# Optimization experiments

Measured on AMD Instinct MI355X. Metric: run time of the kernel, lower is better.

Reference implementation:

```python
import jax, jax.numpy as jnp
import numpy as np

EPS = 1e-5

def _layernorm(x, g, b):
    mu = jnp.mean(x, axis=-1, keepdims=True)
    var = jnp.var(x, axis=-1, keepdims=True)
    return (x - mu) * jax.lax.rsqrt(var + EPS) * g + b

def _pos_encoding(S, D, dtype):
    pos = jnp.arange(S, dtype=jnp.float32)[:, None]
    div = jnp.exp(jnp.arange(0, D, 2, dtype=jnp.float32) * (-jnp.log(10000.0) / D))
    pe = jnp.zeros((S, D), dtype=jnp.float32)
    pe = pe.at[:, 0::2].set(jnp.sin(pos * div))
    pe = pe.at[:, 1::2].set(jnp.cos(pos * div))
    return pe.astype(dtype)

def setup_inputs() -> dict:
    key = jax.random.key(0)
    B, S, D, H, F, L = 4, 1024, 768, 12, 3072, 6
    ks = jax.random.split(key, 8)
    s = 0.02
    return {
        "x": jax.random.normal(ks[0], (B, S, D), jnp.float32),
        "Wqkv": jax.random.normal(ks[1], (L, D, 3 * D), jnp.float32) * s,
        "bqkv": jnp.zeros((L, 3 * D), jnp.float32),
        "Wo": jax.random.normal(ks[2], (L, D, D), jnp.float32) * s,
        "bo": jnp.zeros((L, D), jnp.float32),
        "ln1_g": jnp.ones((L, D), jnp.float32),
        "ln1_b": jnp.zeros((L, D), jnp.float32),
        "W1": jax.random.normal(ks[3], (L, D, F), jnp.float32) * s,
        "b1": jnp.zeros((L, F), jnp.float32),
        "W2": jax.random.normal(ks[4], (L, F, D), jnp.float32) * s,
        "b2": jnp.zeros((L, D), jnp.float32),
        "ln2_g": jnp.ones((L, D), jnp.float32),
        "ln2_b": jnp.zeros((L, D), jnp.float32),
        "lnf_g": jnp.ones((D,), jnp.float32),
        "lnf_b": jnp.zeros((D,), jnp.float32),
        "num_heads": 12,
    }

def reference(x, Wqkv, bqkv, Wo, bo, ln1_g, ln1_b, W1, b1, W2, b2, ln2_g, ln2_b, lnf_g, lnf_b, num_heads):
    B, S, D = x.shape
    H = num_heads
    hd = D // H
    scale = 1.0 / jnp.sqrt(jnp.float32(hd)).astype(x.dtype)

    x = x + _pos_encoding(S, D, x.dtype)[None]

    def layer(h, params):
        wqkv, bq, wo, bo_, g1, b1_, w1, bias1, w2, bias2, g2, b2_ = params
        qkv = (h @ wqkv + bq).reshape(B, S, 3, H, hd)
        q, k, v = jnp.moveaxis(qkv, 2, 0)          # each [B,S,H,hd]
        q = q.transpose(0, 2, 1, 3)                 # bhqd
        k = k.transpose(0, 2, 1, 3)
        v = v.transpose(0, 2, 1, 3)
        scores = jnp.einsum('bhqd,bhkd->bhqk', q, k) * scale
        w = jax.nn.softmax(scores, axis=-1)
        w = jnp.clip(w, 1e-6, 1.0)                  # clamp as in torch module
        attn = jnp.einsum('bhqk,bhkd->bhqd', w, v)
        attn = attn.transpose(0, 2, 1, 3).reshape(B, S, D) @ wo + bo_
        h = _layernorm(h + attn, g1, b1_)
        ffn = jax.nn.relu(h @ w1 + bias1) @ w2 + bias2
        h = _layernorm(h + ffn, g2, b2_)
        return h, None

    params = (Wqkv, bqkv, Wo, bo, ln1_g, ln1_b, W1, b1, W2, b2, ln2_g, ln2_b)
    x, _ = jax.lax.scan(layer, x, params)
    return _layernorm(x, lnf_g, lnf_b)
```

## Files before the change

kernel.cpp:

```cpp
#include <hip/hip_runtime.h>
#include <math.h>

typedef float f32x4 __attribute__((ext_vector_type(4)));
typedef __bf16 bf16x8 __attribute__((ext_vector_type(8)));
typedef unsigned short u16x8 __attribute__((ext_vector_type(8)));

__device__ __forceinline__ unsigned short f2bf(float f) {
    union { float f; unsigned int u; } v; v.f = f;
    unsigned int r = v.u + 0x7FFFu + ((v.u >> 16) & 1u);
    return (unsigned short)(r >> 16);
}
__device__ __forceinline__ float bf2f(unsigned short u) {
    union { unsigned int u; float f; } v; v.u = ((unsigned int)u) << 16;
    return v.f;
}
__device__ __forceinline__ bf16x8 ld8(const unsigned short* p) {
    union { u16x8 u; bf16x8 b; } c;
    c.u = *(const u16x8*)p;
    return c.b;
}
__device__ __forceinline__ void gload_lds16(const unsigned short* g, unsigned short* l) {
    __builtin_amdgcn_global_load_lds(
        (const __attribute__((address_space(1))) unsigned int*)g,
        (__attribute__((address_space(3))) unsigned int*)l,
        16, 0, 0);
}
__device__ __forceinline__ int swz_off(int row, int quad) {
    return row * 32 + ((quad ^ ((row >> 1) & 3)) << 3);
}

__global__ __launch_bounds__(256)
void transpose_convert(const float* __restrict__ W, unsigned short* __restrict__ Wt,
                       int K, int N) {
    __shared__ float tile[32][33];
    int n0 = blockIdx.x * 32, k0 = blockIdx.y * 32;
    int tx = threadIdx.x & 31, ty = threadIdx.x >> 5;
#pragma unroll
    for (int i = 0; i < 4; ++i) {
        int k = ty + i * 8;
        tile[k][tx] = W[(size_t)(k0 + k) * N + n0 + tx];
    }
    __syncthreads();
#pragma unroll
    for (int i = 0; i < 4; ++i) {
        int n = ty + i * 8;
        Wt[(size_t)(n0 + n) * K + k0 + tx] = f2bf(tile[tx][n]);
    }
}

__global__ __launch_bounds__(256)
void posenc_k(const float* __restrict__ x, float* __restrict__ h,
              unsigned short* __restrict__ hb) {
    int idx = blockIdx.x * 256 + threadIdx.x;
    const int TOT = 4 * 1024 * 768;
    if (idx >= TOT) return;
    int d = idx % 768;
    int s = (idx / 768) % 1024;
    int i2 = d >> 1;
    float dv = expf(-(float)(2 * i2) * (9.210340371976184f / 768.0f));
    float ang = (float)s * dv;
    float pe = (d & 1) ? cosf(ang) : sinf(ang);
    float v = x[idx] + pe;
    h[idx] = v;
    hb[idx] = f2bf(v);
}

template<int WF32, int WBF16, int RELU, int BIAS>
__global__ __launch_bounds__(256)
void gemm_k(const unsigned short* __restrict__ A, const unsigned short* __restrict__ Bt,
            const float* __restrict__ bias, float* __restrict__ Cf,
            unsigned short* __restrict__ Cb, int M, int N, int K, int Kc) {
    __shared__ unsigned short As[128 * 32];
    __shared__ unsigned short Bs[128 * 32];
    const int tid = threadIdx.x;
    const int lane = tid & 63, wave = tid >> 6;
    const int l15 = lane & 15, quad = lane >> 4;
    const int m0 = blockIdx.y * 128, n0 = blockIdx.x * 128;
    const int wr = (wave >> 1) * 64, wc = (wave & 1) * 64;
    const int kstart = blockIdx.z * Kc, kend = kstart + Kc;
    float* Cfp = Cf + (size_t)blockIdx.z * M * N;

    const int r0 = wave * 32 + (lane >> 2);
    const int kc0 = lane & 3;

    f32x4 acc[4][4];
#pragma unroll
    for (int i = 0; i < 4; ++i)
#pragma unroll
        for (int j = 0; j < 4; ++j) acc[i][j] = (f32x4){0.f, 0.f, 0.f, 0.f};

    for (int k0 = kstart; k0 < kend; k0 += 32) {
        __syncthreads();
#pragma unroll
        for (int j = 0; j < 2; ++j) {
            int r = r0 + j * 16;
            int kcl = kc0 ^ ((r >> 1) & 3);
            const unsigned short* ga = A + (size_t)(m0 + r) * K + k0 + kcl * 8;
            const unsigned short* gb = Bt + (size_t)(n0 + r) * K + k0 + kcl * 8;
            gload_lds16(ga, &As[(wave * 32 + j * 16) * 32]);
            gload_lds16(gb, &Bs[(wave * 32 + j * 16) * 32]);
        }
        __syncthreads();
        bf16x8 af[4], bfr[4];
#pragma unroll
        for (int mt = 0; mt < 4; ++mt)
            af[mt] = ld8(&As[swz_off(wr + mt * 16 + l15, quad)]);
#pragma unroll
        for (int nt = 0; nt < 4; ++nt)
            bfr[nt] = ld8(&Bs[swz_off(wc + nt * 16 + l15, quad)]);
#pragma unroll
        for (int mt = 0; mt < 4; ++mt)
#pragma unroll
            for (int nt = 0; nt < 4; ++nt)
                acc[mt][nt] = __builtin_amdgcn_mfma_f32_16x16x32_bf16(
                    af[mt], bfr[nt], acc[mt][nt], 0, 0, 0);
    }
#pragma unroll
    for (int mt = 0; mt < 4; ++mt)
#pragma unroll
        for (int nt = 0; nt < 4; ++nt)
#pragma unroll
            for (int r = 0; r < 4; ++r) {
                int row = m0 + wr + mt * 16 + quad * 4 + r;
                int col = n0 + wc + nt * 16 + l15;
                float v = acc[mt][nt][r];
                if (BIAS) v += bias[col];
                if (RELU) v = fmaxf(v, 0.f);
                if (WF32) Cfp[(size_t)row * N + col] = v;
                if (WBF16) Cb[(size_t)row * N + col] = f2bf(v);
            }
}

__global__ __launch_bounds__(256)
void qksplit_k(const unsigned short* __restrict__ qkv, unsigned short* __restrict__ Q,
               unsigned short* __restrict__ Ko) {
    int o8 = blockIdx.x * 256 + threadIdx.x;
    const int NQ8 = 393216;
    int which = (o8 >= NQ8) ? 1 : 0;
    int oo = o8 - which * NQ8;
    int dg = (oo & 7) * 8;
    int s = (oo >> 3) & 1023;
    int bh = oo >> 13;
    int h = bh % 12, b = bh / 12;
    size_t row = (size_t)(b * 1024 + s);
    int col = which * 768 + h * 64 + dg;
    u16x8 val = *(const u16x8*)&qkv[row * 2304 + col];
    if (!which) {
#pragma unroll
        for (int j = 0; j < 8; ++j) val[j] = f2bf(bf2f(val[j]) * 0.125f);
        *(u16x8*)&Q[((size_t)bh * 1024 + s) * 64 + dg] = val;
    } else {
        *(u16x8*)&Ko[((size_t)bh * 1024 + s) * 64 + dg] = val;
    }
}

__global__ __launch_bounds__(256)
void vt_k(const unsigned short* __restrict__ qkv, unsigned short* __restrict__ Vt) {
    __shared__ unsigned short t[64][65];
    int bh = blockIdx.y, s0 = blockIdx.x * 64;
    int b = bh / 12, h = bh % 12;
    int tx = threadIdx.x & 63;
    int ty = threadIdx.x >> 6;
#pragma unroll
    for (int r = 0; r < 16; ++r) {
        int i = ty + r * 4;
        t[i][tx] = qkv[(size_t)(b * 1024 + s0 + i) * 2304 + 1536 + h * 64 + tx];
    }
    __syncthreads();
#pragma unroll
    for (int r = 0; r < 16; ++r) {
        int dd = ty + r * 4;
        Vt[((size_t)bh * 64 + dd) * 1024 + s0 + tx] = t[tx][dd];
    }
}

#define PSTR 68
__global__ __launch_bounds__(256)
void flash_k(const unsigned short* __restrict__ Q, const unsigned short* __restrict__ K,
             const unsigned short* __restrict__ Vt, unsigned short* __restrict__ ctx) {
    const int S = 1024, HD = 64;
    int bh = blockIdx.y;
    int b = bh / 12, h = bh % 12;
    int q0 = blockIdx.x * 64;
    const unsigned short* Qp = Q + ((size_t)bh * S + q0) * HD;
    const unsigned short* Kp = K + (size_t)bh * S * HD;
    const unsigned short* Vp = Vt + (size_t)bh * HD * S;

    __shared__ unsigned short Qs[128 * 32];
    __shared__ unsigned short Ks[128 * 32];
    __shared__ unsigned short Vs[128 * 32];
    __shared__ unsigned short Ps[4 * 16 * PSTR];

    int tid = threadIdx.x;
    int lane = tid & 63, wave = tid >> 6;
    int l15 = lane & 15, quad = lane >> 4;

    const int rl0 = lane >> 2;
    const int c0 = lane & 3;

#pragma unroll
    for (int j = 0; j < 2; ++j) {
        int R = wave * 32 + j * 16 + rl0;
        int khalf = R >> 6, grow = R & 63;
        int lch = c0 ^ ((R >> 1) & 3);
        gload_lds16(Qp + grow * HD + khalf * 32 + lch * 8,
                    &Qs[(wave * 32 + j * 16) * 32]);
    }

    f32x4 o[4];
#pragma unroll
    for (int i = 0; i < 4; ++i) o[i] = (f32x4){0.f, 0.f, 0.f, 0.f};
    float lsum[4] = {0.f, 0.f, 0.f, 0.f};

    unsigned short* Pw = &Ps[wave * 16 * PSTR];

    for (int kt = 0; kt < 16; ++kt) {
        __syncthreads();
#pragma unroll
        for (int j = 0; j < 2; ++j) {
            int R = wave * 32 + j * 16 + rl0;
            int khalf = R >> 6, grow = R & 63;
            int lch = c0 ^ ((R >> 1) & 3);
            gload_lds16(Kp + (kt * 64 + grow) * HD + khalf * 32 + lch * 8,
                        &Ks[(wave * 32 + j * 16) * 32]);
            gload_lds16(Vp + (size_t)grow * S + kt * 64 + khalf * 32 + lch * 8,
                        &Vs[(wave * 32 + j * 16) * 32]);
        }
        __syncthreads();

        bf16x8 qa0 = ld8(&Qs[swz_off(wave * 16 + l15, quad)]);
        bf16x8 qa1 = ld8(&Qs[swz_off(64 + wave * 16 + l15, quad)]);
        f32x4 sc[4];
#pragma unroll
        for (int cb = 0; cb < 4; ++cb) {
            bf16x8 kb0 = ld8(&Ks[swz_off(cb * 16 + l15, quad)]);
            bf16x8 kb1 = ld8(&Ks[swz_off(64 + cb * 16 + l15, quad)]);
            f32x4 z = (f32x4){0.f, 0.f, 0.f, 0.f};
            z = __builtin_amdgcn_mfma_f32_16x16x32_bf16(qa0, kb0, z, 0, 0, 0);
            z = __builtin_amdgcn_mfma_f32_16x16x32_bf16(qa1, kb1, z, 0, 0, 0);
            sc[cb] = z;
        }
#pragma unroll
        for (int cb = 0; cb < 4; ++cb)
#pragma unroll
            for (int r = 0; r < 4; ++r) {
                float pv = __expf(sc[cb][r]);
                sc[cb][r] = pv;
                lsum[r] += pv;
            }
#pragma unroll
        for (int cb = 0; cb < 4; ++cb)
#pragma unroll
            for (int r = 0; r < 4; ++r)
                Pw[(quad * 4 + r) * PSTR + cb * 16 + l15] = f2bf(sc[cb][r]);
        bf16x8 pa0 = ld8(&Pw[l15 * PSTR + quad * 8]);
        bf16x8 pa1 = ld8(&Pw[l15 * PSTR + 32 + quad * 8]);
#pragma unroll
        for (int cb = 0; cb < 4; ++cb) {
            bf16x8 vb0 = ld8(&Vs[swz_off(cb * 16 + l15, quad)]);
            bf16x8 vb1 = ld8(&Vs[swz_off(64 + cb * 16 + l15, quad)]);
            o[cb] = __builtin_amdgcn_mfma_f32_16x16x32_bf16(pa0, vb0, o[cb], 0, 0, 0);
            o[cb] = __builtin_amdgcn_mfma_f32_16x16x32_bf16(pa1, vb1, o[cb], 0, 0, 0);
        }
    }
#pragma unroll
    for (int r = 0; r < 4; ++r) {
#pragma unroll
        for (int off = 1; off < 16; off <<= 1) lsum[r] += __shfl_xor(lsum[r], off);
    }
#pragma unroll
    for (int cb = 0; cb < 4; ++cb)
#pragma unroll
        for (int r = 0; r < 4; ++r) {
            int row = q0 + wave * 16 + quad * 4 + r;
            float val = o[cb][r] / lsum[r];
            ctx[((size_t)(b * 1024 + row)) * 768 + h * 64 + cb * 16 + l15] = f2bf(val);
        }
}

template<int NPART, int WBF16>
__global__ __launch_bounds__(256)
void ln_k(const float* __restrict__ X, const float* __restrict__ P,
          const float* __restrict__ pb,
          const float* __restrict__ g, const float* __restrict__ bta,
          float* __restrict__ Yf, unsigned short* __restrict__ Yb) {
    const int D = 768;
    const size_t MD = (size_t)4096 * 768;
    int row = blockIdx.x;
    int tid = threadIdx.x;
    const float* x = X + (size_t)row * D;
    float v[3];
    float s = 0.f, s2 = 0.f;
#pragma unroll
    for (int i = 0; i < 3; ++i) {
        int c = i * 256 + tid;
        float t = x[c];
        if (NPART > 0) {
            float r = pb[c];
#pragma unroll
            for (int pi = 0; pi < NPART; ++pi)
                r += P[MD * pi + (size_t)row * D + c];
            t += r;
        }
        v[i] = t;
        s += t;
        s2 += t * t;
    }
#pragma unroll
    for (int off = 1; off < 64; off <<= 1) {
        s += __shfl_xor(s, off);
        s2 += __shfl_xor(s2, off);
    }
    __shared__ float rs[4], rs2[4];
    int wave = tid >> 6, lane = tid & 63;
    if (lane == 0) { rs[wave] = s; rs2[wave] = s2; }
    __syncthreads();
    s = rs[0] + rs[1] + rs[2] + rs[3];
    s2 = rs2[0] + rs2[1] + rs2[2] + rs2[3];
    float mu = s * (1.f / 768.f);
    float var = s2 * (1.f / 768.f) - mu * mu;
    float rstd = rsqrtf(var + 1e-5f);
#pragma unroll
    for (int i = 0; i < 3; ++i) {
        int c = i * 256 + tid;
        float y = (v[i] - mu) * rstd * g[c] + bta[c];
        Yf[(size_t)row * D + c] = y;
        if (WBF16) Yb[(size_t)row * D + c] = f2bf(y);
    }
}

extern "C" void kernel_launch(void* const* d_in, const int* in_sizes, int n_in,
                              void* d_out, int out_size, void* d_ws, size_t ws_size,
                              hipStream_t stream) {
    const float* x    = (const float*)d_in[0];
    const float* Wqkv = (const float*)d_in[1];
    const float* bqkv = (const float*)d_in[2];
    const float* Wo   = (const float*)d_in[3];
    const float* bo   = (const float*)d_in[4];
    const float* ln1g = (const float*)d_in[5];
    const float* ln1b = (const float*)d_in[6];
    const float* W1   = (const float*)d_in[7];
    const float* b1   = (const float*)d_in[8];
    const float* W2   = (const float*)d_in[9];
    const float* b2   = (const float*)d_in[10];
    const float* ln2g = (const float*)d_in[11];
    const float* ln2b = (const float*)d_in[12];
    const float* lnfg = (const float*)d_in[13];
    const float* lnfb = (const float*)d_in[14];

    const int B = 4, S = 1024, D = 768, H = 12, F = 3072, L = 6;
    const int M = B * S;

    char* p = (char*)d_ws;
    auto alloc = [&](size_t bytes) -> char* {
        char* r = p;
        p += (bytes + 255) & ~(size_t)255;
        return r;
    };
    float* h             = (float*)alloc((size_t)M * D * 4);
    float* tmp           = (float*)alloc((size_t)4 * M * D * 4);
    unsigned short* hb   = (unsigned short*)alloc((size_t)M * D * 2);
    unsigned short* act  = (unsigned short*)alloc((size_t)M * F * 2);
    unsigned short* Qb   = (unsigned short*)alloc((size_t)M * D * 2);
    unsigned short* Kb   = (unsigned short*)alloc((size_t)M * D * 2);
    unsigned short* Vtb  = (unsigned short*)alloc((size_t)M * D * 2);
    unsigned short* ctx  = (unsigned short*)alloc((size_t)M * D * 2);
    unsigned short* wqkvT = (unsigned short*)alloc((size_t)3 * D * D * 2);
    unsigned short* woT   = (unsigned short*)alloc((size_t)D * D * 2);
    unsigned short* w1T   = (unsigned short*)alloc((size_t)D * F * 2);
    unsigned short* w2T   = (unsigned short*)alloc((size_t)D * F * 2);
    unsigned short* qkvb = act;
    unsigned short* f1b  = act;

    posenc_k<<<(M * D) / 256, 256, 0, stream>>>(x, h, hb);

    for (int l = 0; l < L; ++l) {
        transpose_convert<<<dim3(3 * D / 32, D / 32), 256, 0, stream>>>(
            Wqkv + (size_t)l * D * 3 * D, wqkvT, D, 3 * D);
        transpose_convert<<<dim3(D / 32, D / 32), 256, 0, stream>>>(
            Wo + (size_t)l * D * D, woT, D, D);
        transpose_convert<<<dim3(F / 32, D / 32), 256, 0, stream>>>(
            W1 + (size_t)l * D * F, w1T, D, F);
        transpose_convert<<<dim3(D / 32, F / 32), 256, 0, stream>>>(
            W2 + (size_t)l * F * D, w2T, F, D);

        gemm_k<0, 1, 0, 1><<<dim3(3 * D / 128, M / 128, 1), 256, 0, stream>>>(
            hb, wqkvT, bqkv + (size_t)l * 3 * D, nullptr, qkvb, M, 3 * D, D, D);
        qksplit_k<<<786432 / 256, 256, 0, stream>>>(qkvb, Qb, Kb);
        vt_k<<<dim3(S / 64, B * H), 256, 0, stream>>>(qkvb, Vtb);
        flash_k<<<dim3(S / 64, B * H), 256, 0, stream>>>(Qb, Kb, Vtb, ctx);
        gemm_k<1, 0, 0, 0><<<dim3(D / 128, M / 128, 2), 256, 0, stream>>>(
            ctx, woT, nullptr, tmp, nullptr, M, D, D, D / 2);
        ln_k<2, 1><<<M, 256, 0, stream>>>(h, tmp, bo + (size_t)l * D,
                                          ln1g + (size_t)l * D, ln1b + (size_t)l * D,
                                          h, hb);
        gemm_k<0, 1, 1, 1><<<dim3(F / 128, M / 128, 1), 256, 0, stream>>>(
            hb, w1T, b1 + (size_t)l * F, nullptr, f1b, M, F, D, D);
        gemm_k<1, 0, 0, 0><<<dim3(D / 128, M / 128, 4), 256, 0, stream>>>(
            f1b, w2T, nullptr, tmp, nullptr, M, D, F, F / 4);
        ln_k<4, 1><<<M, 256, 0, stream>>>(h, tmp, b2 + (size_t)l * D,
                                          ln2g + (size_t)l * D, ln2b + (size_t)l * D,
                                          h, hb);
    }
    ln_k<0, 0><<<M, 256, 0, stream>>>(h, nullptr, nullptr, lnfg, lnfb,
                                      (float*)d_out, nullptr);
}
```

Before: 1.393 ms.

## Double-buffer LDS in GEMM and flash attention, store split-K partials as bf16

Adds two-stage LDS double buffering to the GEMM and flash-attention kernels so the next tile's global-to-LDS loads are issued before computing the current tile, with one barrier per iteration. Split-K partial outputs are now written in bf16 instead of fp32, halving partial-sum traffic read by the layernorm kernels. The Wo projection split-K is raised from 2 to 4 for more blocks. This doubles LDS use per block, possibly lowering occupancy, and reduces precision of the residual partial sums.

```diff
diff --git a/kernel.cpp b/kernel.cpp
--- a/kernel.cpp
+++ b/kernel.cpp
@@ -65,49 +65,56 @@
     hb[idx] = f2bf(v);
 }
 
-template<int WF32, int WBF16, int RELU, int BIAS>
+template<int RELU, int BIAS>
 __global__ __launch_bounds__(256)
 void gemm_k(const unsigned short* __restrict__ A, const unsigned short* __restrict__ Bt,
-            const float* __restrict__ bias, float* __restrict__ Cf,
-            unsigned short* __restrict__ Cb, int M, int N, int K, int Kc) {
-    __shared__ unsigned short As[128 * 32];
-    __shared__ unsigned short Bs[128 * 32];
+            const float* __restrict__ bias, unsigned short* __restrict__ Cb,
+            int M, int N, int K, int Kc) {
+    __shared__ unsigned short As[2][128 * 32];
+    __shared__ unsigned short Bs[2][128 * 32];
     const int tid = threadIdx.x;
     const int lane = tid & 63, wave = tid >> 6;
     const int l15 = lane & 15, quad = lane >> 4;
     const int m0 = blockIdx.y * 128, n0 = blockIdx.x * 128;
     const int wr = (wave >> 1) * 64, wc = (wave & 1) * 64;
-    const int kstart = blockIdx.z * Kc, kend = kstart + Kc;
-    float* Cfp = Cf + (size_t)blockIdx.z * M * N;
+    const int kstart = blockIdx.z * Kc;
+    unsigned short* Cbp = Cb + (size_t)blockIdx.z * M * N;
 
     const int r0 = wave * 32 + (lane >> 2);
     const int kc0 = lane & 3;
 
-    f32x4 acc[4][4];
-#pragma unroll
-    for (int i = 0; i < 4; ++i)
-#pragma unroll
-        for (int j = 0; j < 4; ++j) acc[i][j] = (f32x4){0.f, 0.f, 0.f, 0.f};
-
-    for (int k0 = kstart; k0 < kend; k0 += 32) {
-        __syncthreads();
+    auto stage = [&](int k0, int bi) {
 #pragma unroll
         for (int j = 0; j < 2; ++j) {
             int r = r0 + j * 16;
             int kcl = kc0 ^ ((r >> 1) & 3);
-            const unsigned short* ga = A + (size_t)(m0 + r) * K + k0 + kcl * 8;
-            const unsigned short* gb = Bt + (size_t)(n0 + r) * K + k0 + kcl * 8;
-            gload_lds16(ga, &As[(wave * 32 + j * 16) * 32]);
-            gload_lds16(gb, &Bs[(wave * 32 + j * 16) * 32]);
-        }
+            gload_lds16(A + (size_t)(m0 + r) * K + k0 + kcl * 8,
+                        &As[bi][(wave * 32 + j * 16) * 32]);
+            gload_lds16(Bt + (size_t)(n0 + r) * K + k0 + kcl * 8,
+                        &Bs[bi][(wave * 32 + j * 16) * 32]);
+        }
+    };
+
+    f32x4 acc[4][4];
+#pragma unroll
+    for (int i = 0; i < 4; ++i)
+#pragma unroll
+        for (int j = 0; j < 4; ++j) acc[i][j] = (f32x4){0.f, 0.f, 0.f, 0.f};
+
+    stage(kstart, 0);
+    const int nk = Kc / 32;
+    for (int t = 0; t < nk; ++t) {
         __syncthreads();
+        if (t + 1 < nk) stage(kstart + (t + 1) * 32, (t + 1) & 1);
+        const unsigned short* Asb = As[t & 1];
+        const unsigned short* Bsb = Bs[t & 1];
         bf16x8 af[4], bfr[4];
 #pragma unroll
         for (int mt = 0; mt < 4; ++mt)
-            af[mt] = ld8(&As[swz_off(wr + mt * 16 + l15, quad)]);
+            af[mt] = ld8(&Asb[swz_off(wr + mt * 16 + l15, quad)]);
 #pragma unroll
         for (int nt = 0; nt < 4; ++nt)
-            bfr[nt] = ld8(&Bs[swz_off(wc + nt * 16 + l15, quad)]);
+            bfr[nt] = ld8(&Bsb[swz_off(wc + nt * 16 + l15, quad)]);
 #pragma unroll
         for (int mt = 0; mt < 4; ++mt)
 #pragma unroll
@@ -126,8 +133,7 @@
                 float v = acc[mt][nt][r];
                 if (BIAS) v += bias[col];
                 if (RELU) v = fmaxf(v, 0.f);
-                if (WF32) Cfp[(size_t)row * N + col] = v;
-                if (WBF16) Cb[(size_t)row * N + col] = f2bf(v);
+                Cbp[(size_t)row * N + col] = f2bf(v);
             }
 }
 
@@ -187,8 +193,8 @@
     const unsigned short* Vp = Vt + (size_t)bh * HD * S;
 
     __shared__ unsigned short Qs[128 * 32];
-    __shared__ unsigned short Ks[128 * 32];
-    __shared__ unsigned short Vs[128 * 32];
+    __shared__ unsigned short Ks[2][128 * 32];
+    __shared__ unsigned short Vs[2][128 * 32];
     __shared__ unsigned short Ps[4 * 16 * PSTR];
 
     int tid = threadIdx.x;
@@ -197,6 +203,19 @@
 
     const int rl0 = lane >> 2;
     const int c0 = lane & 3;
+
+    auto stageKV = [&](int kt, int bi) {
+#pragma unroll
+        for (int j = 0; j < 2; ++j) {
+            int R = wave * 32 + j * 16 + rl0;
+            int khalf = R >> 6, grow = R & 63;
+            int lch = c0 ^ ((R >> 1) & 3);
+            gload_lds16(Kp + (kt * 64 + grow) * HD + khalf * 32 + lch * 8,
+                        &Ks[bi][(wave * 32 + j * 16) * 32]);
+            gload_lds16(Vp + (size_t)grow * S + kt * 64 + khalf * 32 + lch * 8,
+                        &Vs[bi][(wave * 32 + j * 16) * 32]);
+        }
+    };
 
 #pragma unroll
     for (int j = 0; j < 2; ++j) {
@@ -206,6 +225,7 @@
         gload_lds16(Qp + grow * HD + khalf * 32 + lch * 8,
                     &Qs[(wave * 32 + j * 16) * 32]);
     }
+    stageKV(0, 0);
 
     f32x4 o[4];
 #pragma unroll
@@ -216,25 +236,17 @@
 
     for (int kt = 0; kt < 16; ++kt) {
         __syncthreads();
-#pragma unroll
-        for (int j = 0; j < 2; ++j) {
-            int R = wave * 32 + j * 16 + rl0;
-            int khalf = R >> 6, grow = R & 63;
-            int lch = c0 ^ ((R >> 1) & 3);
-            gload_lds16(Kp + (kt * 64 + grow) * HD + khalf * 32 + lch * 8,
-                        &Ks[(wave * 32 + j * 16) * 32]);
-            gload_lds16(Vp + (size_t)grow * S + kt * 64 + khalf * 32 + lch * 8,
-                        &Vs[(wave * 32 + j * 16) * 32]);
-        }
-        __syncthreads();
+        if (kt < 15) stageKV(kt + 1, (kt + 1) & 1);
+        const unsigned short* Ksb = Ks[kt & 1];
+        const unsigned short* Vsb = Vs[kt & 1];
 
         bf16x8 qa0 = ld8(&Qs[swz_off(wave * 16 + l15, quad)]);
         bf16x8 qa1 = ld8(&Qs[swz_off(64 + wave * 16 + l15, quad)]);
         f32x4 sc[4];
 #pragma unroll
         for (int cb = 0; cb < 4; ++cb) {
-            bf16x8 kb0 = ld8(&Ks[swz_off(cb * 16 + l15, quad)]);
-            bf16x8 kb1 = ld8(&Ks[swz_off(64 + cb * 16 + l15, quad)]);
+            bf16x8 kb0 = ld8(&Ksb[swz_off(cb * 16 + l15, quad)]);
+            bf16x8 kb1 = ld8(&Ksb[swz_off(64 + cb * 16 + l15, quad)]);
             f32x4 z = (f32x4){0.f, 0.f, 0.f, 0.f};
             z = __builtin_amdgcn_mfma_f32_16x16x32_bf16(qa0, kb0, z, 0, 0, 0);
             z = __builtin_amdgcn_mfma_f32_16x16x32_bf16(qa1, kb1, z, 0, 0, 0);
@@ -257,8 +269,8 @@
         bf16x8 pa1 = ld8(&Pw[l15 * PSTR + 32 + quad * 8]);
 #pragma unroll
         for (int cb = 0; cb < 4; ++cb) {
-            bf16x8 vb0 = ld8(&Vs[swz_off(cb * 16 + l15, quad)]);
-            bf16x8 vb1 = ld8(&Vs[swz_off(64 + cb * 16 + l15, quad)]);
+            bf16x8 vb0 = ld8(&Vsb[swz_off(cb * 16 + l15, quad)]);
+            bf16x8 vb1 = ld8(&Vsb[swz_off(64 + cb * 16 + l15, quad)]);
             o[cb] = __builtin_amdgcn_mfma_f32_16x16x32_bf16(pa0, vb0, o[cb], 0, 0, 0);
             o[cb] = __builtin_amdgcn_mfma_f32_16x16x32_bf16(pa1, vb1, o[cb], 0, 0, 0);
         }
@@ -280,7 +292,7 @@
 
 template<int NPART, int WBF16>
 __global__ __launch_bounds__(256)
-void ln_k(const float* __restrict__ X, const float* __restrict__ P,
+void ln_k(const float* __restrict__ X, const unsigned short* __restrict__ P,
           const float* __restrict__ pb,
           const float* __restrict__ g, const float* __restrict__ bta,
           float* __restrict__ Yf, unsigned short* __restrict__ Yb) {
@@ -299,7 +311,7 @@
             float r = pb[c];
 #pragma unroll
             for (int pi = 0; pi < NPART; ++pi)
-                r += P[MD * pi + (size_t)row * D + c];
+                r += bf2f(P[MD * pi + (size_t)row * D + c]);
             t += r;
         }
         v[i] = t;
@@ -358,7 +370,7 @@
         return r;
     };
     float* h             = (float*)alloc((size_t)M * D * 4);
-    float* tmp           = (float*)alloc((size_t)4 * M * D * 4);
+    unsigned short* tmp  = (unsigned short*)alloc((size_t)4 * M * D * 2);
     unsigned short* hb   = (unsigned short*)alloc((size_t)M * D * 2);
     unsigned short* act  = (unsigned short*)alloc((size_t)M * F * 2);
     unsigned short* Qb   = (unsigned short*)alloc((size_t)M * D * 2);
@@ -384,20 +396,20 @@
         transpose_convert<<<dim3(D / 32, F / 32), 256, 0, stream>>>(
             W2 + (size_t)l * F * D, w2T, F, D);
 
-        gemm_k<0, 1, 0, 1><<<dim3(3 * D / 128, M / 128, 1), 256, 0, stream>>>(
-            hb, wqkvT, bqkv + (size_t)l * 3 * D, nullptr, qkvb, M, 3 * D, D, D);
+        gemm_k<0, 1><<<dim3(3 * D / 128, M / 128, 1), 256, 0, stream>>>(
+            hb, wqkvT, bqkv + (size_t)l * 3 * D, qkvb, M, 3 * D, D, D);
         qksplit_k<<<786432 / 256, 256, 0, stream>>>(qkvb, Qb, Kb);
         vt_k<<<dim3(S / 64, B * H), 256, 0, stream>>>(qkvb, Vtb);
         flash_k<<<dim3(S / 64, B * H), 256, 0, stream>>>(Qb, Kb, Vtb, ctx);
-        gemm_k<1, 0, 0, 0><<<dim3(D / 128, M / 128, 2), 256, 0, stream>>>(
-            ctx, woT, nullptr, tmp, nullptr, M, D, D, D / 2);
-        ln_k<2, 1><<<M, 256, 0, stream>>>(h, tmp, bo + (size_t)l * D,
+        gemm_k<0, 0><<<dim3(D / 128, M / 128, 4), 256, 0, stream>>>(
+            ctx, woT, nullptr, tmp, M, D, D, D / 4);
+        ln_k<4, 1><<<M, 256, 0, stream>>>(h, tmp, bo + (size_t)l * D,
                                           ln1g + (size_t)l * D, ln1b + (size_t)l * D,
                                           h, hb);
-        gemm_k<0, 1, 1, 1><<<dim3(F / 128, M / 128, 1), 256, 0, stream>>>(
-            hb, w1T, b1 + (size_t)l * F, nullptr, f1b, M, F, D, D);
-        gemm_k<1, 0, 0, 0><<<dim3(D / 128, M / 128, 4), 256, 0, stream>>>(
-            f1b, w2T, nullptr, tmp, nullptr, M, D, F, F / 4);
+        gemm_k<1, 1><<<dim3(F / 128, M / 128, 1), 256, 0, stream>>>(
+            hb, w1T, b1 + (size_t)l * F, f1b, M, F, D, D);
+        gemm_k<0, 0><<<dim3(D / 128, M / 128, 4), 256, 0, stream>>>(
+            f1b, w2T, nullptr, tmp, M, D, F, F / 4);
         ln_k<4, 1><<<M, 256, 0, stream>>>(h, tmp, b2 + (size_t)l * D,
                                           ln2g + (size_t)l * D, ln2b + (size_t)l * D,
                                           h, hb);
```

Result: faster. 1.319 ms (-5.3%).
